# Optimization experiments

Measured on AMD Instinct MI355X. Metric: run time of the kernel, lower is better.

The kernel has to match this reference:

```python
import jax, jax.numpy as jnp
import numpy as np

B, L = 16, 65536
NUM_BINS = 256
H = 64


def setup_inputs() -> dict:
    key = jax.random.key(0)
    k1, k2, k3, k4 = jax.random.split(key, 4)
    x = jax.random.normal(k1, (B, L), dtype=jnp.float32)
    mask = jax.random.uniform(k4, (B, L)) < 0.1
    x = jnp.where(mask, jnp.nan, x)
    # monotonically increasing bin edges
    bins = jnp.sort(jax.random.normal(k2, (NUM_BINS,), dtype=jnp.float32) * 1.5)
    # nn.Embedding(num_bins + 1, H), default init N(0,1); row 0 is the mask token
    emb_table = jax.random.normal(k3, (NUM_BINS + 1, H), dtype=jnp.float32)
    return {"x": x, "bins": bins, "emb_table": emb_table}


def reference(x, bins, emb_table):
    # BinEmbedding.bin with left_closed=True:
    #   idx = clamp(argmin([x>=b for b in bins] ++ [0]) - 1, min=0)
    # which equals clamp(count(bins <= x) - 1, min=0) = clamp(searchsorted(right) - 1, 0).
    # NaN inputs compare False everywhere in torch -> argmin=0 -> idx=0, then the
    # forward re-injects NaN and DiscreteEmbedding maps NaN -> token 0 (mask).
    nans = jnp.isnan(x)
    xs = jnp.where(nans, jnp.float32(0.0), x)  # sanitize for searchsorted
    idx = jnp.maximum(jnp.searchsorted(bins, xs, side="right") - 1, 0)  # (B, L)
    tok = jnp.where(nans, 0, idx + 1)  # +1 shift; 0 reserved for mask token
    return emb_table[tok]  # (B, L, H)
```

## Files before the change

### kernel.cpp

```cpp
#include <hip/hip_runtime.h>
#include <stdint.h>

#define N_POS (16 * 65536)
#define NBINS 256
#define HDIM  64


typedef float vfloat4 __attribute__((ext_vector_type(4)));

#define POS_PER_BLOCK 256
#define CHUNKS_PER_BLOCK (POS_PER_BLOCK * 16)

__global__ __launch_bounds__(256) void BinEmbedding_49520972923592_kernel(
    const float* __restrict__ x,
    const float* __restrict__ bins,
    const vfloat4* __restrict__ embv,
    vfloat4* __restrict__ out)
{
    __shared__ float s_bins[NBINS];
    __shared__ int   s_tok[POS_PER_BLOCK];

    const int tid = threadIdx.x;
    s_bins[tid] = bins[tid];
    __syncthreads();

    const int pos = blockIdx.x * POS_PER_BLOCK + tid;
    const float xv = x[pos];

    int cnt = 0;
#pragma unroll
    for (int step = 128; step >= 1; step >>= 1) {
        const int cand = cnt + step;
        cnt = (s_bins[cand - 1] <= xv) ? cand : cnt;
    }
    cnt += (s_bins[NBINS - 1] <= xv) ? 1 : 0;

    s_tok[tid] = (xv != xv) ? 0 : (cnt > 0 ? cnt : 1);
    __syncthreads();

    const long base = (long)blockIdx.x * CHUNKS_PER_BLOCK;
#pragma unroll
    for (int i = 0; i < 16; ++i) {
        const int l   = i * 256 + tid;
        const int tok = s_tok[l >> 4];
        const vfloat4 v = embv[tok * 16 + (l & 15)];
        out[base + l] = v;
    }
}

extern "C" void kernel_launch(void* const* d_in, const int* in_sizes, int n_in,
                              void* d_out, int out_size, void* d_ws, size_t ws_size,
                              hipStream_t stream) {
    const float*   x    = (const float*)d_in[0];
    const float*   bins = (const float*)d_in[1];
    const vfloat4* emb  = (const vfloat4*)d_in[2];
    vfloat4* out = (vfloat4*)d_out;

    const dim3 grid(N_POS / POS_PER_BLOCK), block(256);
    hipLaunchKernelGGL(BinEmbedding_49520972923592_kernel, grid, block, 0, stream,
                       x, bins, emb, out);
}
```

Measured before the change: 268.5 us.

## Stage embedding table in LDS and process multiple tiles per block

Copies the whole 257x64 embedding table into shared memory once per block and gathers output rows from LDS rather than global/L2. Each block now handles 8 tiles of 256 positions, using double-buffered token arrays and prefetching the next x value while the current tile is being written. The intent is to cut global gather traffic and per-block setup cost. In exchange, each block uses about 66KB of LDS, which limits occupancy, and there are fewer blocks overall.

```diff
diff --git a/kernel.cpp b/kernel.cpp
--- a/kernel.cpp
+++ b/kernel.cpp
@@ -8,43 +8,58 @@
 
 typedef float vfloat4 __attribute__((ext_vector_type(4)));
 
-#define POS_PER_BLOCK 256
-#define CHUNKS_PER_BLOCK (POS_PER_BLOCK * 16)
+#define THREADS        256
+#define POS_PER_TILE   256
+#define TILES          8
+#define POS_PER_BLOCK  (POS_PER_TILE * TILES)
+#define NBLOCKS        (N_POS / POS_PER_BLOCK)
+#define EMB_ROWS       (NBINS + 1)
+#define EMB_CHUNKS     (EMB_ROWS * 16)
 
-__global__ __launch_bounds__(256) void BinEmbedding_49520972923592_kernel(
+__global__ __launch_bounds__(THREADS, 2)
+void BinEmbedding_49520972923592_kernel(
     const float* __restrict__ x,
     const float* __restrict__ bins,
     const vfloat4* __restrict__ embv,
     vfloat4* __restrict__ out)
 {
-    __shared__ float s_bins[NBINS];
-    __shared__ int   s_tok[POS_PER_BLOCK];
+    __shared__ vfloat4 s_emb[EMB_CHUNKS];
+    __shared__ float   s_bins[NBINS];
+    __shared__ int     s_tok[2][POS_PER_TILE];
 
     const int tid = threadIdx.x;
+
     s_bins[tid] = bins[tid];
+    for (int c = tid; c < EMB_CHUNKS; c += THREADS)
+        s_emb[c] = embv[c];
+
+    const long pbase = (long)blockIdx.x * POS_PER_BLOCK;
+    float xv = x[pbase + tid];
     __syncthreads();
 
-    const int pos = blockIdx.x * POS_PER_BLOCK + tid;
-    const float xv = x[pos];
+    for (int tile = 0; tile < TILES; ++tile) {
+        int cnt = 0;
+#pragma unroll
+        for (int step = 128; step >= 1; step >>= 1) {
+            const int cand = cnt + step;
+            cnt = (s_bins[cand - 1] <= xv) ? cand : cnt;
+        }
+        cnt += (s_bins[NBINS - 1] <= xv) ? 1 : 0;
 
-    int cnt = 0;
+        s_tok[tile & 1][tid] = (xv != xv) ? 0 : (cnt > 0 ? cnt : 1);
+
+        if (tile + 1 < TILES)
+            xv = x[pbase + (tile + 1) * POS_PER_TILE + tid];
+
+        __syncthreads();
+
+        const int* st = s_tok[tile & 1];
+        const long cbase = (pbase + (long)tile * POS_PER_TILE) * 16;
 #pragma unroll
-    for (int step = 128; step >= 1; step >>= 1) {
-        const int cand = cnt + step;
-        cnt = (s_bins[cand - 1] <= xv) ? cand : cnt;
-    }
-    cnt += (s_bins[NBINS - 1] <= xv) ? 1 : 0;
-
-    s_tok[tid] = (xv != xv) ? 0 : (cnt > 0 ? cnt : 1);
-    __syncthreads();
-
-    const long base = (long)blockIdx.x * CHUNKS_PER_BLOCK;
-#pragma unroll
-    for (int i = 0; i < 16; ++i) {
-        const int l   = i * 256 + tid;
-        const int tok = s_tok[l >> 4];
-        const vfloat4 v = embv[tok * 16 + (l & 15)];
-        out[base + l] = v;
+        for (int i = 0; i < 16; ++i) {
+            const int l = i * THREADS + tid;
+            out[cbase + l] = s_emb[st[l >> 4] * 16 + (l & 15)];
+        }
     }
 }
 
@@ -56,7 +71,7 @@
     const vfloat4* emb  = (const vfloat4*)d_in[2];
     vfloat4* out = (vfloat4*)d_out;
 
-    const dim3 grid(N_POS / POS_PER_BLOCK), block(256);
+    const dim3 grid(NBLOCKS), block(THREADS);
     hipLaunchKernelGGL(BinEmbedding_49520972923592_kernel, grid, block, 0, stream,
                        x, bins, emb, out);
 }
```

Measured after the change: 271.9 us. About the same (+1.3%).
